# Kernel tuning notes

Measured on AMD Instinct MI355X. Metric: run time of the kernel, lower is better.

## Reference

```python
import jax, jax.numpy as jnp
import numpy as np

EPS = 1e-8  # torch.cosine_similarity default eps


def _gelu(x):
    # torch nn.GELU default = exact (erf) gelu
    return jax.nn.gelu(x, approximate=False)


def setup_inputs() -> dict:
    key = jax.random.key(0)
    ks = jax.random.split(key, 12)
    B, D, H1, E, N, K = 32768, 768, 256, 128, 500, 5
    TOT = D + E + 1 + 1 + 4  # 902, importance_net input dim
    s = 0.02
    return {
        "cue": jax.random.normal(ks[0], (B, D), jnp.float32),
        "internal_state": jnp.zeros((B, E), jnp.float32),
        "reward": jax.random.uniform(ks[1], (B, 1), dtype=jnp.float32),
        "timestamp": jax.random.uniform(ks[2], (B, 1), dtype=jnp.float32),
        "emotional_state": jax.random.uniform(ks[3], (B, 4), dtype=jnp.float32),
        "centroids": jax.random.normal(ks[4], (N, E), jnp.float32),
        "enc_w1": jax.random.normal(ks[5], (D, H1), jnp.float32) * s,
        "enc_b1": jnp.zeros((H1,), jnp.float32),
        "enc_w2": jax.random.normal(ks[6], (H1, E), jnp.float32) * s,
        "enc_b2": jnp.zeros((E,), jnp.float32),
        "imp_w1": jax.random.normal(ks[7], (TOT, 64), jnp.float32) * s,
        "imp_b1": jnp.zeros((64,), jnp.float32),
        "imp_w2": jax.random.normal(ks[8], (64, 1), jnp.float32) * s,
        "imp_b2": jnp.zeros((1,), jnp.float32),
        "top_k": K,
    }


def reference(cue, internal_state, reward, timestamp, emotional_state, centroids,
              enc_w1, enc_b1, enc_w2, enc_b2,
              imp_w1, imp_b1, imp_w2, imp_b2, top_k):
    # --- encoder MLP (batched over all cues instead of per-item calls) ---
    enc = _gelu(cue @ enc_w1 + enc_b1) @ enc_w2 + enc_b2        # [B, 128]

    # --- cosine similarity vs all cluster centroids (fused loop) ---
    num = enc @ centroids.T                                      # [B, N]
    e_n = jnp.linalg.norm(enc, axis=-1, keepdims=True)           # [B, 1]
    c_n = jnp.linalg.norm(centroids, axis=-1)                    # [N]
    sims = num / jnp.maximum(e_n * c_n[None, :], EPS)            # [B, N]
    top_vals, _ = jax.lax.top_k(sims, top_k)                     # [B, K]

    # --- importance net on combined memory entry ---
    combined = jnp.concatenate(
        [cue, internal_state, reward, timestamp, emotional_state], axis=-1)  # [B, 902]
    imp = jax.nn.sigmoid(_gelu(combined @ imp_w1 + imp_b1) @ imp_w2 + imp_b2)  # [B, 1]
    imp = imp * jnp.mean(emotional_state, axis=-1, keepdims=True)

    return jnp.concatenate([top_vals, imp], axis=-1)             # [B, K+1]
```

## Files before the change

### kernel.cpp

```cpp
#include <hip/hip_runtime.h>
#include <hip/hip_bf16.h>
#include <hip/hip_fp16.h>
#include <math.h>

using f32x4  = __attribute__((ext_vector_type(4))) float;
using half8  = __attribute__((ext_vector_type(8))) _Float16;
using uint4v = __attribute__((ext_vector_type(4))) unsigned int;

#define WAITV(N) asm volatile("s_waitcnt vmcnt(" #N ")" ::: "memory")
#define LGKM0    asm volatile("s_waitcnt lgkmcnt(0)" ::: "memory")

__device__ __forceinline__ unsigned short f32_to_f16u(float f) {
  return __half_as_ushort(__float2half(f));
}
__device__ __forceinline__ float f16u_to_f32(unsigned short h) {
  return __half2float(__ushort_as_half(h));
}
__device__ __forceinline__ unsigned int pk2(float a, float b) {
  return (unsigned int)f32_to_f16u(a) | ((unsigned int)f32_to_f16u(b) << 16);
}
__device__ __forceinline__ f32x4 mfma16(half8 a, half8 b, f32x4 c) {
  return __builtin_amdgcn_mfma_f32_16x16x32_f16(a, b, c, 0, 0, 0);
}
__device__ __forceinline__ void gload_lds16(void* lds, const void* g) {
  __builtin_amdgcn_global_load_lds(
      (const __attribute__((address_space(1))) unsigned int*)g,
      (__attribute__((address_space(3))) unsigned int*)lds, 16, 0, 0);
}
__device__ __forceinline__ float gelu_exact(float x) {
  return 0.5f * x * (1.0f + erff(x * 0.70710678118654752440f));
}


__global__ __launch_bounds__(256) void k_prep(
    const float* __restrict__ enc_w1, const float* __restrict__ enc_w2,
    const float* __restrict__ imp_w1, const float* __restrict__ cent,
    const float* __restrict__ reward, const float* __restrict__ tsp,
    const float* __restrict__ emo,
    unsigned short* __restrict__ W1T, unsigned short* __restrict__ W2T,
    unsigned short* __restrict__ impW1T, unsigned short* __restrict__ centC,
    float* __restrict__ c_n, unsigned short* __restrict__ tail) {
  __shared__ float ld[64][65];
  const int bx = blockIdx.x, t = threadIdx.x;
  if (bx < 48) {
    int tk = bx % 12, tn = bx / 12;
    int k0 = tk * 64, n0 = tn * 64;
    int cn = t & 63, r4 = t >> 6;
#pragma unroll
    for (int pass = 0; pass < 16; ++pass) {
      int kk = pass * 4 + r4;
      ld[kk][cn] = enc_w1[(size_t)(k0 + kk) * 256 + n0 + cn];
    }
    __syncthreads();
    int ck = t & 63, rn4 = t >> 6;
#pragma unroll
    for (int pass = 0; pass < 16; ++pass) {
      int nn = pass * 4 + rn4;
      W1T[(size_t)(n0 + nn) * 768 + k0 + ck] = f32_to_f16u(ld[ck][nn]);
    }
    return;
  }
  int idx = (bx - 48) * 256 + t;
  if (idx < 128 * 256) {
    int n = idx >> 8, k = idx & 255;
    W2T[idx] = f32_to_f16u(enc_w2[k * 128 + n]);
  }
  if (idx < 64 * 960) {
    int n = idx / 960, k = idx - n * 960;
    impW1T[idx] = (k < 902) ? f32_to_f16u(imp_w1[k * 64 + n]) : (unsigned short)0;
  }
  if (idx < 512 * 128) {
    int n = idx >> 7, k = idx & 127;
    centC[idx] = (n < 500) ? f32_to_f16u(cent[n * 128 + k]) : (unsigned short)0;
  }
  if (idx < 512) {
    float s = 0.f;
    if (idx < 500) {
      const f32x4* p = (const f32x4*)(cent + idx * 128);
#pragma unroll 8
      for (int j = 0; j < 32; ++j) {
        f32x4 v = p[j];
#pragma unroll
        for (int e = 0; e < 4; ++e) {
          float q = (float)(_Float16)v[e];
          s += q * q;
        }
      }
    }
    c_n[idx] = sqrtf(s);
  }
  if (idx < 32768) {
    f32x4 e4 = *(const f32x4*)(emo + (size_t)idx * 4);
    unsigned short* tp = tail + (size_t)idx * 8;
    tp[0] = f32_to_f16u(reward[idx]);
    tp[1] = f32_to_f16u(tsp[idx]);
    tp[2] = f32_to_f16u(e4[0]); tp[3] = f32_to_f16u(e4[1]);
    tp[4] = f32_to_f16u(e4[2]); tp[5] = f32_to_f16u(e4[3]);
    tp[6] = 0; tp[7] = 0;
  }
}

__global__ __launch_bounds__(512, 4) void k_fused(
    const float* __restrict__ cue, const float* __restrict__ internal,
    const float* __restrict__ emo,
    const unsigned short* __restrict__ W1T, const unsigned short* __restrict__ impW1T,
    const unsigned short* __restrict__ tail,
    const unsigned short* __restrict__ W2T, const unsigned short* __restrict__ centC,
    const float* __restrict__ c_n,
    const float* __restrict__ b1, const float* __restrict__ b2,
    const float* __restrict__ ib1, const float* __restrict__ iw2,
    const float* __restrict__ ib2, float* __restrict__ out) {
  __shared__ unsigned char sm[73728];
  const int t = threadIdx.x;
  const int lane = t & 63, w = t >> 6;
  const int wr = w >> 2, wc = w & 3;
  const int g = lane >> 4, c = lane & 15;
  const int row0 = blockIdx.x * 64;

  const int srow = t >> 3, q8 = t & 7;
  const int abyte = srow * 128 + q8 * 16;
  const int aswz = (srow & 7) << 4;
  const int myrow = row0 + srow;

  f32x4 aLo, aHi;
  auto issueA = [&](int j) {
    const float* s = (j < 12)
        ? (cue + (size_t)myrow * 768 + j * 64 + q8 * 8)
        : (internal + (size_t)myrow * 128 + (j - 12) * 64 + q8 * 8);
    aLo = *(const f32x4*)s;
    aHi = *(const f32x4*)(s + 4);
  };
  auto convWrite = [&](int buf) {
    uint4v u = {pk2(aLo[0], aLo[1]), pk2(aLo[2], aLo[3]),
                pk2(aHi[0], aHi[1]), pk2(aHi[2], aHi[3])};
    *(uint4v*)(sm + buf * 8192 + (abyte ^ aswz)) = u;
  };
  auto issueB1 = [&](int j) {
#pragma unroll
    for (int i = 0; i < 4; ++i) {
      int L = i * 8192 + t * 16;
      int nl = L >> 7, x = L & 127;
      gload_lds16(sm + 24576 + i * 8192 + w * 1024,
                  (const unsigned char*)W1T + ((size_t)nl * 768 + j * 64) * 2 +
                      (x ^ ((nl & 7) << 4)));
    }
  };
  auto issueB2 = [&](int j, int buf) {
    int L = t * 16, nl = L >> 7, x = L & 127;
    gload_lds16(sm + 57344 + buf * 8192 + w * 1024,
                (const unsigned char*)impW1T + (size_t)nl * 1920 + j * 128 +
                    (x ^ ((nl & 7) << 4)));
  };

  f32x4 acc1[2][4];
  f32x4 acc2[2];
#pragma unroll
  for (int i = 0; i < 2; ++i) {
    acc2[i] = f32x4{0.f, 0.f, 0.f, 0.f};
#pragma unroll
    for (int j = 0; j < 4; ++j) acc1[i][j] = f32x4{0.f, 0.f, 0.f, 0.f};
  }

  auto mfma_step = [&](int abuf, int b2buf, bool enc) {
    const unsigned char* Ab  = sm + abuf * 8192;
    const unsigned char* Bb2 = sm + 57344 + b2buf * 8192;
#pragma unroll
    for (int ks = 0; ks < 2; ++ks) {
      half8 af[2];
#pragma unroll
      for (int mf = 0; mf < 2; ++mf) {
        int m = wr * 32 + mf * 16 + c;
        af[mf] = *(const half8*)(Ab + m * 128 + ((ks * 64 + g * 16) ^ ((m & 7) << 4)));
      }
      {
        int n2 = wc * 16 + c;
        half8 b2f = *(const half8*)(Bb2 + n2 * 128 + ((ks * 64 + g * 16) ^ ((n2 & 7) << 4)));
        acc2[0] = mfma16(af[0], b2f, acc2[0]);
        acc2[1] = mfma16(af[1], b2f, acc2[1]);
      }
      if (enc) {
#pragma unroll
        for (int nf = 0; nf < 4; ++nf) {
          int n = wc * 64 + nf * 16 + c;
          half8 bf = *(const half8*)(sm + 24576 + n * 128 +
                                     ((ks * 64 + g * 16) ^ ((n & 7) << 4)));
          acc1[0][nf] = mfma16(af[0], bf, acc1[0][nf]);
          acc1[1][nf] = mfma16(af[1], bf, acc1[1][nf]);
        }
      }
    }
  };

  {
    uint4v tl = {0u, 0u, 0u, 0u};
    if (q8 == 0) tl = *(const uint4v*)(tail + (size_t)myrow * 8);
    issueA(0); issueB1(0); issueB2(0, 0);
    *(uint4v*)(sm + 16384 + (abyte ^ aswz)) = tl;
    convWrite(0);
    issueA(1); issueB2(1, 1);
    WAITV(3);
    LGKM0;
    __builtin_amdgcn_s_barrier();
  }

  int p = 0;
  for (int it = 0; it < 12; ++it) {
    mfma_step(p, p, true);
    convWrite(p ^ 1);
    LGKM0;
    __builtin_amdgcn_s_barrier();
    if (it < 11) issueB1(it + 1);
    issueA(it + 2);
    issueB2(it + 2, p);
    WAITV(3);
    __builtin_amdgcn_s_barrier();
    p ^= 1;
  }
  mfma_step(0, 0, false);
  convWrite(1);
  LGKM0;
  __builtin_amdgcn_s_barrier();
  issueB2(14, 0);
  WAITV(1);
  __builtin_amdgcn_s_barrier();
  mfma_step(1, 1, false);
  LGKM0;
  __builtin_amdgcn_s_barrier();
  WAITV(0);
  __builtin_amdgcn_s_barrier();
  mfma_step(2, 0, false);

  float* s_pn = (float*)(sm + 65536);
  float* s_en = (float*)(sm + 67584);
  float* s_p  = (float*)(sm + 67840);
  unsigned int* s_mk = (unsigned int*)(sm + 68864);

  __syncthreads();

  {
    float b1v = ib1[wc * 16 + c];
    float w2v = iw2[wc * 16 + c];
#pragma unroll
    for (int mf = 0; mf < 2; ++mf)
#pragma unroll
      for (int rr = 0; rr < 4; ++rr) {
        float v = gelu_exact(acc2[mf][rr] + b1v) * w2v;
        v += __shfl_xor(v, 1);
        v += __shfl_xor(v, 2);
        v += __shfl_xor(v, 4);
        v += __shfl_xor(v, 8);
        if (c == 0) s_p[(wr * 32 + mf * 16 + g * 4 + rr) * 4 + wc] = v;
      }
    float bias1[4];
#pragma unroll
    for (int nf = 0; nf < 4; ++nf) bias1[nf] = b1[wc * 64 + nf * 16 + c];
#pragma unroll
    for (int mf = 0; mf < 2; ++mf)
#pragma unroll
      for (int nf = 0; nf < 4; ++nf)
#pragma unroll
        for (int rr = 0; rr < 4; ++rr) {
          int row = wr * 32 + mf * 16 + g * 4 + rr;
          int col = wc * 64 + nf * 16 + c;
          float x = gelu_exact(acc1[mf][nf][rr] + bias1[nf]);
          *(unsigned short*)(sm + row * 512 + ((col * 2) ^ ((row & 7) << 4))) =
              f32_to_f16u(x);
        }
  }
  __syncthreads();

  if (t < 64) {
    float ssum = s_p[t * 4 + 0] + s_p[t * 4 + 1] + s_p[t * 4 + 2] + s_p[t * 4 + 3];
    int rowA = row0 + t;
    float z = ssum + ib2[0];
    float sig = 1.0f / (1.0f + expf(-z));
    f32x4 e4 = *(const f32x4*)(emo + (size_t)rowA * 4);
    float m4 = 0.25f * (e4[0] + e4[1] + e4[2] + e4[3]);
    out[(size_t)rowA * 6 + 5] = sig * m4;
  }

  f32x4 acc_e[4];
#pragma unroll
  for (int mf = 0; mf < 4; ++mf) acc_e[mf] = f32x4{0.f, 0.f, 0.f, 0.f};
#pragma unroll
  for (int kh = 0; kh < 2; ++kh) {
#pragma unroll
    for (int i = 0; i < 4; ++i) {
      int L = i * 8192 + t * 16;
      int nl = L >> 8, x = L & 255;
      gload_lds16(sm + 32768 + i * 8192 + w * 1024,
                  (const unsigned char*)W2T + (size_t)nl * 512 + kh * 256 +
                      (x ^ ((nl & 7) << 4)));
    }
    __syncthreads();
#pragma unroll
    for (int ks = 0; ks < 4; ++ks) {
      half8 af[4];
#pragma unroll
      for (int mf = 0; mf < 4; ++mf) {
        int m = mf * 16 + c;
        af[mf] = *(const half8*)(sm + m * 512 +
                                 ((kh * 256 + ks * 64 + g * 16) ^ ((m & 7) << 4)));
      }
      int nl = w * 16 + c;
      half8 bf = *(const half8*)(sm + 32768 + nl * 256 +
                                 ((ks * 64 + g * 16) ^ ((nl & 7) << 4)));
#pragma unroll
      for (int mf = 0; mf < 4; ++mf) acc_e[mf] = mfma16(af[mf], bf, acc_e[mf]);
    }
    __syncthreads();
  }

  {
    float bias2 = b2[w * 16 + c];
#pragma unroll
    for (int mf = 0; mf < 4; ++mf)
#pragma unroll
      for (int rr = 0; rr < 4; ++rr) {
        int row = mf * 16 + g * 4 + rr;
        float x = acc_e[mf][rr] + bias2;
        unsigned short hv = f32_to_f16u(x);
        float xr = f16u_to_f32(hv);
        *(unsigned short*)(sm + row * 256 + (((w * 16 + c) * 2) ^ ((row & 7) << 4))) = hv;
        float v = xr * xr;
        v += __shfl_xor(v, 1);
        v += __shfl_xor(v, 2);
        v += __shfl_xor(v, 4);
        v += __shfl_xor(v, 8);
        if (c == 0) s_pn[row * 8 + w] = v;
      }
  }
  __syncthreads();
  if (t < 64) {
    float s = 0.f;
#pragma unroll
    for (int i = 0; i < 8; ++i) s += s_pn[t * 8 + i];
    s_en[t] = sqrtf(s);
  }
  __syncthreads();

  const int rlb = (w & 3) * 16;
  const int halfsel = w >> 2;
  float en[4];
#pragma unroll
  for (int r = 0; r < 4; ++r) en[r] = s_en[rlb + g * 4 + r];
  half8 af2[4];
  {
    int rl = rlb + c;
#pragma unroll
    for (int kk = 0; kk < 4; ++kk)
      af2[kk] = *(const half8*)(sm + rl * 256 +
                                ((kk * 64 + g * 16) ^ ((rl & 7) << 4)));
  }

  unsigned int top5[4][5];
#pragma unroll
  for (int r = 0; r < 4; ++r)
#pragma unroll
    for (int s5 = 0; s5 < 5; ++s5) top5[r][s5] = 0u;

#pragma unroll
  for (int ch = 0; ch < 4; ++ch) {
    __syncthreads();
#pragma unroll
    for (int i = 0; i < 4; ++i) {
      int L = i * 8192 + t * 16;
      int nl = L >> 8, x = L & 255;
      gload_lds16(sm + 32768 + i * 8192 + w * 1024,
                  (const unsigned char*)centC + (size_t)(ch * 128 + nl) * 256 +
                      (x ^ ((nl & 7) << 4)));
    }
    __syncthreads();
#pragma unroll
    for (int nfc = 0; nfc < 4; ++nfc) {
      int nl = halfsel * 64 + nfc * 16 + c;
      const unsigned char* bbase = sm + 32768 + nl * 256;
      int swz = (nl & 7) << 4;
      f32x4 acc = f32x4{0.f, 0.f, 0.f, 0.f};
#pragma unroll
      for (int kk = 0; kk < 4; ++kk) {
        half8 bf = *(const half8*)(bbase + ((kk * 64 + g * 16) ^ swz));
        acc = mfma16(af2[kk], bf, acc);
      }
      int col = ch * 128 + nl;
      float cnv = c_n[col];
#pragma unroll
      for (int r = 0; r < 4; ++r) {
        float denom = fmaxf(en[r] * cnv, 1e-8f);
        float v = acc[r] * __builtin_amdgcn_rcpf(denom);
        unsigned int u = __float_as_uint(v);
        u = (u & 0x80000000u) ? ~u : (u | 0x80000000u);
        unsigned int k = (col < 500) ? ((u & 0xFFFFFE00u) | (unsigned)col) : 0u;
        unsigned int t0 = top5[r][0], t1 = top5[r][1], t2 = top5[r][2],
                     t3 = top5[r][3], t4 = top5[r][4];
        top5[r][0] = (k > t0) ? k : t0;
        top5[r][1] = (k > t0) ? t0 : ((k > t1) ? k : t1);
        top5[r][2] = (k > t1) ? t1 : ((k > t2) ? k : t2);
        top5[r][3] = (k > t2) ? t2 : ((k > t3) ? k : t3);
        top5[r][4] = (k > t3) ? t3 : ((k > t4) ? k : t4);
      }
    }
  }

#pragma unroll
  for (int r = 0; r < 4; ++r) {
    int row = rlb + g * 4 + r;
    unsigned int h0 = top5[r][0], h1v = top5[r][1], h2 = top5[r][2],
                 h3 = top5[r][3], h4 = top5[r][4];
#pragma unroll
    for (int it5 = 0; it5 < 5; ++it5) {
      unsigned int best = h0;
#pragma unroll
      for (int s = 1; s < 16; s <<= 1) {
        unsigned int o = __shfl_xor(best, s);
        best = (o > best) ? o : best;
      }
      if (c == 0) s_mk[(row * 2 + halfsel) * 5 + it5] = best;
      bool pop = (h0 == best);
      h0 = pop ? h1v : h0;
      h1v = pop ? h2 : h1v;
      h2 = pop ? h3 : h2;
      h3 = pop ? h4 : h3;
      h4 = pop ? 0u : h4;
    }
  }
  __syncthreads();

  if (t < 64) {
    const unsigned int* A = s_mk + (t * 2 + 0) * 5;
    const unsigned int* B = s_mk + (t * 2 + 1) * 5;
    int ia = 0, ib = 0;
#pragma unroll
    for (int o = 0; o < 5; ++o) {
      unsigned int a = (ia < 5) ? A[ia] : 0u;
      unsigned int b = (ib < 5) ? B[ib] : 0u;
      unsigned int best;
      if (a >= b) { best = a; ++ia; } else { best = b; ++ib; }
      unsigned int m = best & 0xFFFFFE00u;
      unsigned int uu = (m & 0x80000000u) ? (m ^ 0x80000000u) : ~m;
      out[(size_t)(row0 + t) * 6 + o] = __uint_as_float(uu);
    }
  }
}

extern "C" void kernel_launch(void* const* d_in, const int* in_sizes, int n_in,
                              void* d_out, int out_size, void* d_ws, size_t ws_size,
                              hipStream_t stream) {
  (void)in_sizes; (void)n_in; (void)out_size; (void)ws_size;
  const float* cue      = (const float*)d_in[0];
  const float* internal = (const float*)d_in[1];
  const float* reward   = (const float*)d_in[2];
  const float* tsp      = (const float*)d_in[3];
  const float* emo      = (const float*)d_in[4];
  const float* cent     = (const float*)d_in[5];
  const float* enc_w1   = (const float*)d_in[6];
  const float* enc_b1   = (const float*)d_in[7];
  const float* enc_w2   = (const float*)d_in[8];
  const float* enc_b2   = (const float*)d_in[9];
  const float* imp_w1   = (const float*)d_in[10];
  const float* imp_b1   = (const float*)d_in[11];
  const float* imp_w2   = (const float*)d_in[12];
  const float* imp_b2   = (const float*)d_in[13];
  float* out = (float*)d_out;

  unsigned char* ws = (unsigned char*)d_ws;
  unsigned short* W1T    = (unsigned short*)(ws + 0);
  unsigned short* W2T    = (unsigned short*)(ws + 393216);
  unsigned short* impW1T = (unsigned short*)(ws + 458752);
  unsigned short* centC  = (unsigned short*)(ws + 581632);
  float*          c_n    = (float*)(ws + 712704);
  unsigned short* tail   = (unsigned short*)(ws + 714752);

  k_prep<<<304, 256, 0, stream>>>(enc_w1, enc_w2, imp_w1, cent, reward, tsp, emo,
                                  W1T, W2T, impW1T, centC, c_n, tail);
  k_fused<<<512, 512, 0, stream>>>(cue, internal, emo, W1T, impW1T, tail,
                                   W2T, centC, c_n, enc_b1, enc_b2,
                                   imp_b1, imp_w2, imp_b2, out);
}
```

Measured before the change: 63.13 us.

## Prefetch W2 and double-buffer centroid chunks to overlap loads with epilogue MFMAs

Restructures the tail of the kernel so global-to-LDS loads overlap with compute. The first W2 half is now issued during the last main-loop MFMA step and the second half during the first encoder-output MFMA pass. The centroid tiles are split into 64-column chunks held in two LDS buffers, with the next chunk prefetched while the current one is processed. Full __syncthreads are replaced with explicit vmcnt/lgkmcnt waits plus raw barriers, which adds risk of LDS buffer aliasing races if the counts or buffer offsets are wrong.

Measured after the change: 68.95 us. 1.09x slower.

```diff
diff --git a/kernel.cpp b/kernel.cpp
--- a/kernel.cpp
+++ b/kernel.cpp
@@ -9,6 +9,7 @@
 
 #define WAITV(N) asm volatile("s_waitcnt vmcnt(" #N ")" ::: "memory")
 #define LGKM0    asm volatile("s_waitcnt lgkmcnt(0)" ::: "memory")
+#define SBAR     __builtin_amdgcn_s_barrier()
 
 __device__ __forceinline__ unsigned short f32_to_f16u(float f) {
   return __half_as_ushort(__float2half(f));
@@ -151,6 +152,26 @@
                 (const unsigned char*)impW1T + (size_t)nl * 1920 + j * 128 +
                     (x ^ ((nl & 7) << 4)));
   };
+  auto issueW2T = [&](int kh) {
+#pragma unroll
+    for (int i = 0; i < 4; ++i) {
+      int L = i * 8192 + t * 16;
+      int nl = L >> 8, x = L & 255;
+      gload_lds16(sm + 32768 + i * 8192 + w * 1024,
+                  (const unsigned char*)W2T + (size_t)nl * 512 + kh * 256 +
+                      (x ^ ((nl & 7) << 4)));
+    }
+  };
+  auto issueC = [&](int ch, int buf) {
+#pragma unroll
+    for (int i = 0; i < 2; ++i) {
+      int L = i * 8192 + t * 16;
+      int nl = L >> 8, x = L & 255;
+      gload_lds16(sm + 16384 + buf * 16384 + i * 8192 + w * 1024,
+                  (const unsigned char*)centC + (size_t)(ch * 64 + nl) * 256 +
+                      (x ^ ((nl & 7) << 4)));
+    }
+  };
 
   f32x4 acc1[2][4];
   f32x4 acc2[2];
@@ -200,7 +221,7 @@
     issueA(1); issueB2(1, 1);
     WAITV(3);
     LGKM0;
-    __builtin_amdgcn_s_barrier();
+    SBAR;
   }
 
   int p = 0;
@@ -208,34 +229,34 @@
     mfma_step(p, p, true);
     convWrite(p ^ 1);
     LGKM0;
-    __builtin_amdgcn_s_barrier();
+    SBAR;
     if (it < 11) issueB1(it + 1);
     issueA(it + 2);
     issueB2(it + 2, p);
     WAITV(3);
-    __builtin_amdgcn_s_barrier();
+    SBAR;
     p ^= 1;
   }
   mfma_step(0, 0, false);
   convWrite(1);
   LGKM0;
-  __builtin_amdgcn_s_barrier();
-  issueB2(14, 0);
-  WAITV(1);
-  __builtin_amdgcn_s_barrier();
+  WAITV(0);
+  SBAR;
   mfma_step(1, 1, false);
   LGKM0;
-  __builtin_amdgcn_s_barrier();
-  WAITV(0);
-  __builtin_amdgcn_s_barrier();
-  mfma_step(2, 0, false);
+  SBAR;
+  issueB2(14, 1);
+  issueW2T(0);
+  WAITV(4);
+  SBAR;
+  mfma_step(2, 1, false);
+  LGKM0;
+  SBAR;
 
   float* s_pn = (float*)(sm + 65536);
   float* s_en = (float*)(sm + 67584);
   float* s_p  = (float*)(sm + 67840);
   unsigned int* s_mk = (unsigned int*)(sm + 68864);
-
-  __syncthreads();
 
   {
     float b1v = ib1[wc * 16 + c];
@@ -267,8 +288,30 @@
               f32_to_f16u(x);
         }
   }
-  __syncthreads();
-
+  WAITV(0);
+  LGKM0;
+  SBAR;
+
+  f32x4 acc_e[4];
+#pragma unroll
+  for (int mf = 0; mf < 4; ++mf) acc_e[mf] = f32x4{0.f, 0.f, 0.f, 0.f};
+#pragma unroll
+  for (int ks = 0; ks < 4; ++ks) {
+    half8 af[4];
+#pragma unroll
+    for (int mf = 0; mf < 4; ++mf) {
+      int m = mf * 16 + c;
+      af[mf] = *(const half8*)(sm + m * 512 + ((ks * 64 + g * 16) ^ ((m & 7) << 4)));
+    }
+    int nl = w * 16 + c;
+    half8 bf = *(const half8*)(sm + 32768 + nl * 256 +
+                               ((ks * 64 + g * 16) ^ ((nl & 7) << 4)));
+#pragma unroll
+    for (int mf = 0; mf < 4; ++mf) acc_e[mf] = mfma16(af[mf], bf, acc_e[mf]);
+  }
+  LGKM0;
+  SBAR;
+  issueW2T(1);
   if (t < 64) {
     float ssum = s_p[t * 4 + 0] + s_p[t * 4 + 1] + s_p[t * 4 + 2] + s_p[t * 4 + 3];
     int rowA = row0 + t;
@@ -278,38 +321,25 @@
     float m4 = 0.25f * (e4[0] + e4[1] + e4[2] + e4[3]);
     out[(size_t)rowA * 6 + 5] = sig * m4;
   }
-
-  f32x4 acc_e[4];
-#pragma unroll
-  for (int mf = 0; mf < 4; ++mf) acc_e[mf] = f32x4{0.f, 0.f, 0.f, 0.f};
-#pragma unroll
-  for (int kh = 0; kh < 2; ++kh) {
-#pragma unroll
-    for (int i = 0; i < 4; ++i) {
-      int L = i * 8192 + t * 16;
-      int nl = L >> 8, x = L & 255;
-      gload_lds16(sm + 32768 + i * 8192 + w * 1024,
-                  (const unsigned char*)W2T + (size_t)nl * 512 + kh * 256 +
-                      (x ^ ((nl & 7) << 4)));
-    }
-    __syncthreads();
-#pragma unroll
-    for (int ks = 0; ks < 4; ++ks) {
-      half8 af[4];
-#pragma unroll
-      for (int mf = 0; mf < 4; ++mf) {
-        int m = mf * 16 + c;
-        af[mf] = *(const half8*)(sm + m * 512 +
-                                 ((kh * 256 + ks * 64 + g * 16) ^ ((m & 7) << 4)));
-      }
-      int nl = w * 16 + c;
-      half8 bf = *(const half8*)(sm + 32768 + nl * 256 +
-                                 ((ks * 64 + g * 16) ^ ((nl & 7) << 4)));
-#pragma unroll
-      for (int mf = 0; mf < 4; ++mf) acc_e[mf] = mfma16(af[mf], bf, acc_e[mf]);
-    }
-    __syncthreads();
-  }
+  WAITV(1);
+  SBAR;
+#pragma unroll
+  for (int ks = 0; ks < 4; ++ks) {
+    half8 af[4];
+#pragma unroll
+    for (int mf = 0; mf < 4; ++mf) {
+      int m = mf * 16 + c;
+      af[mf] = *(const half8*)(sm + m * 512 +
+                               ((256 + ks * 64 + g * 16) ^ ((m & 7) << 4)));
+    }
+    int nl = w * 16 + c;
+    half8 bf = *(const half8*)(sm + 32768 + nl * 256 +
+                               ((ks * 64 + g * 16) ^ ((nl & 7) << 4)));
+#pragma unroll
+    for (int mf = 0; mf < 4; ++mf) acc_e[mf] = mfma16(af[mf], bf, acc_e[mf]);
+  }
+  LGKM0;
+  SBAR;
 
   {
     float bias2 = b2[w * 16 + c];
@@ -330,14 +360,18 @@
         if (c == 0) s_pn[row * 8 + w] = v;
       }
   }
-  __syncthreads();
+  LGKM0;
+  SBAR;
+  issueC(0, 0);
   if (t < 64) {
     float s = 0.f;
 #pragma unroll
     for (int i = 0; i < 8; ++i) s += s_pn[t * 8 + i];
     s_en[t] = sqrtf(s);
   }
-  __syncthreads();
+  WAITV(0);
+  LGKM0;
+  SBAR;
 
   const int rlb = (w & 3) * 16;
   const int halfsel = w >> 2;
@@ -360,21 +394,13 @@
     for (int s5 = 0; s5 < 5; ++s5) top5[r][s5] = 0u;
 
 #pragma unroll
-  for (int ch = 0; ch < 4; ++ch) {
-    __syncthreads();
-#pragma unroll
-    for (int i = 0; i < 4; ++i) {
-      int L = i * 8192 + t * 16;
-      int nl = L >> 8, x = L & 255;
-      gload_lds16(sm + 32768 + i * 8192 + w * 1024,
-                  (const unsigned char*)centC + (size_t)(ch * 128 + nl) * 256 +
-                      (x ^ ((nl & 7) << 4)));
-    }
-    __syncthreads();
-#pragma unroll
-    for (int nfc = 0; nfc < 4; ++nfc) {
-      int nl = halfsel * 64 + nfc * 16 + c;
-      const unsigned char* bbase = sm + 32768 + nl * 256;
+  for (int ch = 0; ch < 8; ++ch) {
+    if (ch < 7) issueC(ch + 1, (ch + 1) & 1);
+    const unsigned char* Cb = sm + 16384 + (ch & 1) * 16384;
+#pragma unroll
+    for (int nfc = 0; nfc < 2; ++nfc) {
+      int nl = halfsel * 32 + nfc * 16 + c;
+      const unsigned char* bbase = Cb + nl * 256;
       int swz = (nl & 7) << 4;
       f32x4 acc = f32x4{0.f, 0.f, 0.f, 0.f};
 #pragma unroll
@@ -382,7 +408,7 @@
         half8 bf = *(const half8*)(bbase + ((kk * 64 + g * 16) ^ swz));
         acc = mfma16(af2[kk], bf, acc);
       }
-      int col = ch * 128 + nl;
+      int col = ch * 64 + nl;
       float cnv = c_n[col];
 #pragma unroll
       for (int r = 0; r < 4; ++r) {
@@ -400,6 +426,10 @@
         top5[r][4] = (k > t3) ? t3 : ((k > t4) ? k : t4);
       }
     }
+    if (ch < 7) {
+      WAITV(0);
+      SBAR;
+    }
   }
 
 #pragma unroll
@@ -424,7 +454,8 @@
       h4 = pop ? 0u : h4;
     }
   }
-  __syncthreads();
+  LGKM0;
+  SBAR;
 
   if (t < 64) {
     const unsigned int* A = s_mk + (t * 2 + 0) * 5;
```
